# Optimization experiments

Hardware: AMD Instinct MI355X
Metric: run time of the kernel (lower is better)

The kernel has to match this reference:

```python
import jax, jax.numpy as jnp
import numpy as np

N_NODES = 100000
N_EDGES = 1600000
IN_C, HID, OUT_C = 16, 64, 1


def setup_inputs() -> dict:
    key = jax.random.key(0)
    ks = jax.random.split(key, 12)
    x = jax.random.normal(ks[0], (N_NODES, IN_C), dtype=jnp.float32)
    edge_index = jax.random.randint(ks[1], (2, N_EDGES), 0, N_NODES, dtype=jnp.int32)

    def lin(k, fan_in, fan_out):
        s = 1.0 / np.sqrt(fan_in)
        kw, kb = jax.random.split(k)
        W = jax.random.uniform(kw, (fan_in, fan_out), jnp.float32, -s, s)
        b = jax.random.uniform(kb, (fan_out,), jnp.float32, -s, s)
        return W, b

    W0, b0 = lin(ks[2], IN_C, HID)      # node_mlps[0]
    W1, b1 = lin(ks[3], HID, HID)       # node_mlps[1]
    W2, b2 = lin(ks[4], HID, OUT_C)     # node_mlps[2]
    M0, bM0 = lin(ks[5], 2 * HID, HID)  # message_mlps[0] (only one used for num_layers=3)
    return {"x": x, "edge_index": edge_index, "W0": W0, "b0": b0,
            "W1": W1, "b1": b1, "W2": W2, "b2": b2, "M0": M0, "bM0": bM0}


def _message_passing(h, src, dst, M, bM):
    # gather -> concat -> linear -> scatter-add -> degree normalize
    msgs = jnp.concatenate([h[src], h[dst]], axis=1) @ M + bM  # [E, HID]
    agg = jax.ops.segment_sum(msgs, dst, num_segments=N_NODES)  # [N, HID]
    deg = jax.ops.segment_sum(jnp.ones((src.shape[0],), h.dtype), dst,
                              num_segments=N_NODES)
    deg = jnp.clip(deg, 1.0, None)[:, None]
    return agg / deg


def reference(x, edge_index, W0, b0, W1, b1, W2, b2, M0, bM0):
    src, dst = edge_index[0], edge_index[1]
    h = jax.nn.relu(x @ W0 + b0)                  # node_mlps[0] (dropout = eval identity)
    h = h + _message_passing(h, src, dst, M0, bM0)
    h = jax.nn.relu(h @ W1 + b1)                  # node_mlps[1]
    return h @ W2 + b2                            # node_mlps[2], [N, 1]
```

## Files before the change

kernel.cpp:

```cpp
#include <hip/hip_runtime.h>

#define HID 64
#define IN_C 16

typedef __attribute__((ext_vector_type(8))) short short8;
typedef __attribute__((ext_vector_type(4))) float f32x4;

__device__ __forceinline__ float bitsf(unsigned u) { return __uint_as_float(u); }
__device__ __forceinline__ unsigned rne16(float f) {
    unsigned u = __float_as_uint(f);
    return (u + 0x7fffu + ((u >> 16) & 1u)) >> 16;
}
__device__ __forceinline__ float lanebcf(float v, int l) {
    return __int_as_float(__builtin_amdgcn_readlane(__float_as_int(v), l));
}
__device__ __forceinline__ float f4c(const float4& a, int c) {
    switch (c & 3) { case 0: return a.x; case 1: return a.y; case 2: return a.z; default: return a.w; }
}

__global__ void k_init(const float* __restrict__ M0, const float* __restrict__ W1,
                       const float* __restrict__ bM0, const float* __restrict__ b1,
                       ushort* __restrict__ WPhi, ushort* __restrict__ WPlo,
                       float* __restrict__ bias192) {
    int tid = blockIdx.x * 256 + threadIdx.x;
    if (tid >= 64 * 192) return;
    int cc = tid % 192;
    int k  = tid / 192;
    float w;
    if (cc < 64) {
        float a = 0.f;
#pragma unroll
        for (int m = 0; m < HID; ++m) a = fmaf(M0[k * HID + m], W1[m * HID + cc], a);
        w = a;
    } else if (cc < 128) {
        int c = cc - 64;
        float a = W1[k * HID + c];
#pragma unroll
        for (int m = 0; m < HID; ++m) a = fmaf(M0[(HID + k) * HID + m], W1[m * HID + c], a);
        w = a;
    } else {
        w = W1[k * HID + (cc - 128)];
    }
    unsigned wb = __float_as_uint(w);
    ushort hi = (ushort)(wb >> 16);
    float hif = __uint_as_float(wb & 0xffff0000u);
    ushort lo = (ushort)(__float_as_uint(w - hif) >> 16);
    int ct = cc >> 4, s = k >> 5, l = ((k >> 3) & 3) * 16 + (cc & 15), j = k & 7;
    int fi = ((ct * 2 + s) * 64 + l) * 8 + j;
    WPhi[fi] = hi;
    WPlo[fi] = lo;
    if (k == 0) {
        float bv;
        if (cc < 64) bv = 0.f;
        else if (cc < 128) {
            int c = cc - 64;
            float a = b1[c];
#pragma unroll
            for (int m = 0; m < HID; ++m) a = fmaf(bM0[m], W1[m * HID + c], a);
            bv = a;
        } else bv = b1[cc - 128];
        bias192[cc] = bv;
    }
}

__global__ __launch_bounds__(256) void k_pre_hist(
    const float* __restrict__ x, const float* __restrict__ W0, const float* __restrict__ b0,
    const ushort* __restrict__ WPhi, const ushort* __restrict__ WPlo,
    const float* __restrict__ bias192,
    ushort* __restrict__ zb, float* __restrict__ PQ, ushort* __restrict__ Ppb, int N,
    const int* __restrict__ ei, int* __restrict__ bhT, int E, int B1, int NB1)
{
    __shared__ ushort hhi[64 * 64];
    __shared__ ushort hlo[64 * 64];

    if ((int)blockIdx.x < NB1) {
        int* h = reinterpret_cast<int*>(hhi);
        for (int i = threadIdx.x; i < B1; i += 256) h[i] = 0;
        __syncthreads();
        int CH = (E + NB1 - 1) / NB1;
        int e0 = blockIdx.x * CH;
        int e1 = min(e0 + CH, E);
        for (int e = e0 + (int)threadIdx.x; e < e1; e += 256)
            atomicAdd(&h[ei[E + e] >> 8], 1);
        __syncthreads();
        for (int i = threadIdx.x; i < B1; i += 256)
            bhT[(size_t)i * NB1 + blockIdx.x] = h[i];
        return;
    }

    int tid  = threadIdx.x;
    int lane = tid & 63;
    int w    = tid >> 6;
    int n0   = (blockIdx.x - NB1) * 64;

    float w0c[IN_C];
#pragma unroll
    for (int k = 0; k < IN_C; ++k) w0c[k] = W0[k * HID + lane];
    float b0l = b0[lane];

    short8 Whi[3][2], Wlo[3][2];
    float4 bias4[3];
#pragma unroll
    for (int i = 0; i < 3; ++i) {
        int ct = w * 3 + i;
#pragma unroll
        for (int s = 0; s < 2; ++s) {
            int fi = ((ct * 2 + s) * 64 + lane) * 8;
            Whi[i][s] = *reinterpret_cast<const short8*>(WPhi + fi);
            Wlo[i][s] = *reinterpret_cast<const short8*>(WPlo + fi);
        }
        bias4[i] = *reinterpret_cast<const float4*>(bias192 + ct * 16 + (lane >> 4) * 4);
    }

    int nx = n0 + w * 16 + (lane >> 2);
    float4 xq = make_float4(0.f, 0.f, 0.f, 0.f);
    if (nx < N) xq = *reinterpret_cast<const float4*>(x + (size_t)nx * IN_C + (lane & 3) * 4);

#pragma unroll
    for (int nn = 0; nn < 16; ++nn) {
        float acc = b0l;
#pragma unroll
        for (int k = 0; k < IN_C; ++k)
            acc = fmaf(lanebcf(f4c(xq, k & 3), 4 * nn + (k >> 2)), w0c[k], acc);
        float h = fmaxf(acc, 0.f);
        unsigned hb = __float_as_uint(h);
        ushort hi = (ushort)(hb >> 16);
        float hif = __uint_as_float(hb & 0xffff0000u);
        ushort lo = (ushort)(__float_as_uint(h - hif) >> 16);
        int nl = w * 16 + nn;
        int u  = ((lane >> 3) ^ (nl & 7));
        int off = nl * 64 + u * 8 + (lane & 7);
        hhi[off] = hi;
        hlo[off] = lo;
    }
    __syncthreads();

#pragma unroll
    for (int st = 0; st < 4; ++st) {
        int nloc = st * 16 + (lane & 15);
        short8 Ahi[2], Alo[2];
#pragma unroll
        for (int s = 0; s < 2; ++s) {
            int u = (s * 4 + (lane >> 4)) ^ (nloc & 7);
            int off = nloc * 64 + u * 8;
            Ahi[s] = *reinterpret_cast<const short8*>(hhi + off);
            Alo[s] = *reinterpret_cast<const short8*>(hlo + off);
        }
        int n = n0 + st * 16 + (lane & 15);
#pragma unroll
        for (int i = 0; i < 3; ++i) {
            int ct = w * 3 + i;
            f32x4 acc = {bias4[i].x, bias4[i].y, bias4[i].z, bias4[i].w};
#pragma unroll
            for (int s = 0; s < 2; ++s) {
                acc = __builtin_amdgcn_mfma_f32_16x16x32_bf16(Whi[i][s], Ahi[s], acc, 0, 0, 0);
                acc = __builtin_amdgcn_mfma_f32_16x16x32_bf16(Whi[i][s], Alo[s], acc, 0, 0, 0);
                acc = __builtin_amdgcn_mfma_f32_16x16x32_bf16(Wlo[i][s], Ahi[s], acc, 0, 0, 0);
                acc = __builtin_amdgcn_mfma_f32_16x16x32_bf16(Wlo[i][s], Alo[s], acc, 0, 0, 0);
            }
            if (n < N) {
                int chb = ct * 16 + (lane >> 4) * 4;
                if (chb < 64) {
                    uint2 pk;
                    pk.x = rne16(acc[0]) | (rne16(acc[1]) << 16);
                    pk.y = rne16(acc[2]) | (rne16(acc[3]) << 16);
                    *reinterpret_cast<uint2*>(zb + (size_t)n * HID + chb) = pk;
                } else if (chb < 128) {
                    float4 v = make_float4(acc[0], acc[1], acc[2], acc[3]);
                    *reinterpret_cast<float4*>(PQ + (size_t)n * HID + (chb - 64)) = v;
                } else {
                    uint2 pk;
                    pk.x = rne16(acc[0]) | (rne16(acc[1]) << 16);
                    pk.y = rne16(acc[2]) | (rne16(acc[3]) << 16);
                    *reinterpret_cast<uint2*>(Ppb + (size_t)n * HID + (chb - 128)) = pk;
                }
            }
        }
    }
}

__global__ void k_scan1(const int* __restrict__ cnt, int* __restrict__ rs,
                        int* __restrict__ bsum, int M) {
    __shared__ int lds[256];
    int t = threadIdx.x;
    int base = blockIdx.x * 4096 + t * 16;
    int v[16];
    if (base + 16 <= M) {
#pragma unroll
        for (int u = 0; u < 4; ++u) {
            int4 w = *reinterpret_cast<const int4*>(cnt + base + u * 4);
            v[u * 4 + 0] = w.x; v[u * 4 + 1] = w.y; v[u * 4 + 2] = w.z; v[u * 4 + 3] = w.w;
        }
    } else {
#pragma unroll
        for (int u = 0; u < 16; ++u) v[u] = (base + u < M) ? cnt[base + u] : 0;
    }
    int run = 0;
#pragma unroll
    for (int u = 0; u < 16; ++u) { int tv = v[u]; v[u] = run; run += tv; }
    lds[t] = run;
    __syncthreads();
#pragma unroll
    for (int off = 1; off < 256; off <<= 1) {
        int xw = (t >= off) ? lds[t - off] : 0;
        __syncthreads();
        lds[t] += xw;
        __syncthreads();
    }
    int excl = lds[t] - run;
    if (t == 255) bsum[blockIdx.x] = lds[255];
#pragma unroll
    for (int u = 0; u < 16; ++u)
        if (base + u < M) rs[base + u] = excl + v[u];
}

__global__ __launch_bounds__(256) void k_p1scat(const int* __restrict__ ei, const int* __restrict__ off,
                                                const int* __restrict__ bsum, int NBs,
                                                unsigned* __restrict__ tmp, int E, int B1) {
    __shared__ int cur[1024];
    __shared__ int lds[256];
    __shared__ int excl[256];
    int NB1 = gridDim.x;
    int t = threadIdx.x;
    int v = (t < NBs) ? bsum[t] : 0;
    lds[t] = v;
    __syncthreads();
#pragma unroll
    for (int o = 1; o < 256; o <<= 1) {
        int xw = (t >= o) ? lds[t - o] : 0;
        __syncthreads();
        lds[t] += xw;
        __syncthreads();
    }
    excl[t] = lds[t] - v;
    __syncthreads();
    for (int i = t; i < B1; i += 256) {
        int idx = i * NB1 + blockIdx.x;
        cur[i] = off[idx] + excl[idx >> 12];
    }
    __syncthreads();
    int CH = (E + NB1 - 1) / NB1;
    int e0 = blockIdx.x * CH;
    int e1 = min(e0 + CH, E);
    for (int e = e0 + t; e < e1; e += 256) {
        int s = ei[e];
        int d = ei[E + e];
        int pos = atomicAdd(&cur[d >> 8], 1);
        tmp[pos] = (unsigned)s | ((unsigned)(d & 255) << 24);
    }
}

__global__ __launch_bounds__(256) void k_p2(const unsigned* __restrict__ tmp, const int* __restrict__ off,
                                            const int* __restrict__ bsum, int NBs,
                                            int* __restrict__ rs, int* __restrict__ csr,
                                            int E, int N, int B1, int NB1) {
    __shared__ int h2[256];
    __shared__ int sc[256];
    __shared__ int cur[256];
    __shared__ int bb[2];
    int b = blockIdx.x;
    int t = threadIdx.x;

    {
        int v = (t < NBs) ? bsum[t] : 0;
        sc[t] = v;
        __syncthreads();
#pragma unroll
        for (int o = 1; o < 256; o <<= 1) {
            int xw = (t >= o) ? sc[t - o] : 0;
            __syncthreads();
            sc[t] += xw;
            __syncthreads();
        }
        if (t == 0) {
            int i0 = b * NB1;
            bb[0] = off[i0] + (sc[i0 >> 12] - ((i0 >> 12) < NBs ? bsum[i0 >> 12] : 0));
        } else if (t == 1 && b < B1 - 1) {
            int i1 = (b + 1) * NB1;
            bb[1] = off[i1] + (sc[i1 >> 12] - ((i1 >> 12) < NBs ? bsum[i1 >> 12] : 0));
        } else if (t == 1) {
            bb[1] = E;
        }
    }
    __syncthreads();
    int bb0 = bb[0];
    int bb1 = bb[1];

    h2[t] = 0;
    __syncthreads();
    for (int i = bb0 + t; i < bb1; i += 256)
        atomicAdd(&h2[tmp[i] >> 24], 1);
    __syncthreads();

    int v = h2[t];
    sc[t] = v;
    __syncthreads();
#pragma unroll
    for (int o = 1; o < 256; o <<= 1) {
        int xw = (t >= o) ? sc[t - o] : 0;
        __syncthreads();
        sc[t] += xw;
        __syncthreads();
    }
    int excl = sc[t] - v;

    int node = b * 256 + t;
    if (node < N) rs[node] = bb0 + excl;
    if (b == B1 - 1 && t == 0) rs[N] = E;
    cur[t] = bb0 + excl;
    __syncthreads();

    for (int i = bb0 + t; i < bb1; i += 256) {
        unsigned ed = tmp[i];
        int pos = atomicAdd(&cur[ed >> 24], 1);
        csr[pos] = (int)(ed & 0x00FFFFFFu);
    }
}

__global__ __launch_bounds__(256) void k_final(
    const ushort* __restrict__ zb, const float* __restrict__ PQ, const ushort* __restrict__ Ppb,
    const int* __restrict__ rs, const int* __restrict__ csr,
    const float* __restrict__ W2, const float* __restrict__ b2,
    float* __restrict__ out, int N)
{
    int lane = threadIdx.x & 63;
    int g    = lane >> 4;
    int ql   = lane & 15;
    int oct  = ql & 7;
    int half = ql >> 3;
    int wid  = (blockIdx.x * 256 + threadIdx.x) >> 6;
    int nw   = (gridDim.x * 256) >> 6;

    int c0 = oct * 8 + half * 4;
    float4 w2v = *reinterpret_cast<const float4*>(W2 + c0);
    float b2s = b2[0];

    for (int n0 = wid * 4; n0 < N; n0 += nw * 4) {
        int ng   = n0 + g;
        bool okg = ng < N;

        int rv = okg ? rs[ng + half] : 0;
        int beg = __shfl(rv, g * 16 + 0);
        int end = __shfl(rv, g * 16 + 8);
        int deg = end - beg;
        int md = deg;
        md = max(md, __shfl_xor(md, 16));
        md = max(md, __shfl_xor(md, 32));

        float acc[8];
#pragma unroll
        for (int i = 0; i < 8; ++i) acc[i] = 0.f;

        for (int c = 0; c < md; c += 32) {
            int j0 = c + ql, j1 = c + 16 + ql;
            int ia = (j0 < deg) ? csr[beg + j0] : -1;
            int ib = (j1 < deg) ? csr[beg + j1] : -1;
#pragma unroll
            for (int tb = 0; tb < 4; ++tb) {
                if (tb > 0 && md <= c + 8 * tb) break;
                int srcs[4];
#pragma unroll
                for (int t4 = 0; t4 < 4; ++t4) {
                    int t = tb * 4 + t4;
                    int e = 2 * t + half;
                    srcs[t4] = __shfl(tb < 2 ? ia : ib, g * 16 + (e & 15));
                }
                uint4 rw[4];
#pragma unroll
                for (int t4 = 0; t4 < 4; ++t4) {
                    int s = srcs[t4] < 0 ? 0 : srcs[t4];
                    rw[t4] = *reinterpret_cast<const uint4*>(zb + (size_t)s * HID + oct * 8);
                }
#pragma unroll
                for (int t4 = 0; t4 < 4; ++t4) {
                    if (srcs[t4] >= 0) {
                        uint4 wv = rw[t4];
                        acc[0] += bitsf(wv.x << 16); acc[1] += bitsf(wv.x & 0xffff0000u);
                        acc[2] += bitsf(wv.y << 16); acc[3] += bitsf(wv.y & 0xffff0000u);
                        acc[4] += bitsf(wv.z << 16); acc[5] += bitsf(wv.z & 0xffff0000u);
                        acc[6] += bitsf(wv.w << 16); acc[7] += bitsf(wv.w & 0xffff0000u);
                    }
                }
            }
        }
#pragma unroll
        for (int i = 0; i < 8; ++i) acc[i] += __shfl_xor(acc[i], 8);

        float s0 = half ? acc[4] : acc[0];
        float s1 = half ? acc[5] : acc[1];
        float s2 = half ? acc[6] : acc[2];
        float s3 = half ? acc[7] : acc[3];

        float4 base = make_float4(0.f, 0.f, 0.f, 0.f);
        if (okg) {
            base = *reinterpret_cast<const float4*>(PQ + (size_t)ng * HID + c0);
            if (deg == 0) {
                uint2 pb = *reinterpret_cast<const uint2*>(Ppb + (size_t)ng * HID + c0);
                base.x = bitsf(pb.x << 16); base.y = bitsf(pb.x & 0xffff0000u);
                base.z = bitsf(pb.y << 16); base.w = bitsf(pb.y & 0xffff0000u);
            }
        }
        float rcpd = (deg > 0) ? (1.f / (float)deg) : 0.f;
        float y0 = base.x + s0 * rcpd;
        float y1 = base.y + s1 * rcpd;
        float y2 = base.z + s2 * rcpd;
        float y3 = base.w + s3 * rcpd;

        float part = fmaxf(y0, 0.f) * w2v.x + fmaxf(y1, 0.f) * w2v.y +
                     fmaxf(y2, 0.f) * w2v.z + fmaxf(y3, 0.f) * w2v.w;
#pragma unroll
        for (int off = 1; off < 16; off <<= 1) part += __shfl_xor(part, off);
        if (ql == 0 && okg) out[ng] = part + b2s;
    }
}

extern "C" void kernel_launch(void* const* d_in, const int* in_sizes, int n_in,
                              void* d_out, int out_size, void* d_ws, size_t ws_size,
                              hipStream_t stream) {
    const float* x   = (const float*)d_in[0];
    const int*   ei  = (const int*)d_in[1];
    const float* W0  = (const float*)d_in[2];
    const float* b0  = (const float*)d_in[3];
    const float* W1  = (const float*)d_in[4];
    const float* b1  = (const float*)d_in[5];
    const float* W2  = (const float*)d_in[6];
    const float* b2  = (const float*)d_in[7];
    const float* M0  = (const float*)d_in[8];
    const float* bM0 = (const float*)d_in[9];

    int N = in_sizes[0] / IN_C;
    int E = in_sizes[1] / 2;
    int B1 = (N + 255) >> 8;
    int NB1 = 256;
    int M2 = B1 * NB1;
    int NBs = (M2 + 4095) / 4096;

    ushort*   zb     = (ushort*)d_ws;
    float*    PQ     = (float*)(zb + (size_t)N * HID);
    ushort*   Ppb    = (ushort*)(PQ + (size_t)N * HID);
    ushort*   WPhi   = Ppb + (size_t)N * HID;
    ushort*   WPlo   = WPhi + 12288;
    float*    bias192= (float*)(WPlo + 12288);
    int*      bhT    = (int*)(bias192 + 192);
    int*      off    = bhT + (size_t)M2;
    int*      bsum   = off + (size_t)M2;
    int*      rs     = bsum + 256;
    unsigned* tmp    = (unsigned*)(rs + N + 1);
    int*      csr    = (int*)(tmp + (size_t)E);
    float*    out    = (float*)d_out;

    int npre = (N + 63) / 64;

    k_init<<<48, 256, 0, stream>>>(M0, W1, bM0, b1, WPhi, WPlo, bias192);
    k_pre_hist<<<NB1 + npre, 256, 0, stream>>>(x, W0, b0, WPhi, WPlo, bias192,
                                               zb, PQ, Ppb, N, ei, bhT, E, B1, NB1);
    k_scan1<<<NBs, 256, 0, stream>>>(bhT, off, bsum, M2);
    k_p1scat<<<NB1, 256, 0, stream>>>(ei, off, bsum, NBs, tmp, E, B1);
    k_p2<<<B1, 256, 0, stream>>>(tmp, off, bsum, NBs, rs, csr, E, N, B1, NB1);
    k_final<<<2048, 256, 0, stream>>>(zb, PQ, Ppb, rs, csr, W2, b2, out, N);
}
```

Measured before the change: 101.8 us.

## Fuse CSR fine-sort into final aggregation with 64-node buckets and LDS-resident CSR

Shrinks the destination buckets from 256 to 64 nodes and merges the second-pass sort kernel with the final aggregation kernel. Each block now sorts its bucket's edges into a shared-memory CSR and consumes them directly, with a global-memory fallback when a bucket holds more than LCAP edges. The aim is to cut one launch and the global write and re-read of the row-start and CSR arrays. In exchange, the fused grid has fewer blocks than the old final kernel, and each block serializes its sort phase before aggregation.

```diff
diff --git a/kernel.cpp b/kernel.cpp
--- a/kernel.cpp
+++ b/kernel.cpp
@@ -2,6 +2,8 @@
 
 #define HID 64
 #define IN_C 16
+#define BKT 64
+#define LCAP 2048
 
 typedef __attribute__((ext_vector_type(8))) short short8;
 typedef __attribute__((ext_vector_type(4))) float f32x4;
@@ -81,7 +83,7 @@
         int e0 = blockIdx.x * CH;
         int e1 = min(e0 + CH, E);
         for (int e = e0 + (int)threadIdx.x; e < e1; e += 256)
-            atomicAdd(&h[ei[E + e] >> 8], 1);
+            atomicAdd(&h[ei[E + e] >> 6], 1);
         __syncthreads();
         for (int i = threadIdx.x; i < B1; i += 256)
             bhT[(size_t)i * NB1 + blockIdx.x] = h[i];
@@ -217,7 +219,7 @@
 __global__ __launch_bounds__(256) void k_p1scat(const int* __restrict__ ei, const int* __restrict__ off,
                                                 const int* __restrict__ bsum, int NBs,
                                                 unsigned* __restrict__ tmp, int E, int B1) {
-    __shared__ int cur[1024];
+    __shared__ int cur[2048];
     __shared__ int lds[256];
     __shared__ int excl[256];
     int NB1 = gridDim.x;
@@ -245,19 +247,26 @@
     for (int e = e0 + t; e < e1; e += 256) {
         int s = ei[e];
         int d = ei[E + e];
-        int pos = atomicAdd(&cur[d >> 8], 1);
-        tmp[pos] = (unsigned)s | ((unsigned)(d & 255) << 24);
-    }
-}
-
-__global__ __launch_bounds__(256) void k_p2(const unsigned* __restrict__ tmp, const int* __restrict__ off,
-                                            const int* __restrict__ bsum, int NBs,
-                                            int* __restrict__ rs, int* __restrict__ csr,
-                                            int E, int N, int B1, int NB1) {
-    __shared__ int h2[256];
+        int pos = atomicAdd(&cur[d >> 6], 1);
+        tmp[pos] = (unsigned)s | ((unsigned)(d & 63) << 26);
+    }
+}
+
+__global__ __launch_bounds__(256) void k_p2f(
+    const unsigned* __restrict__ tmp, const int* __restrict__ off,
+    const int* __restrict__ bsum, int NBs,
+    const ushort* __restrict__ zb, const float* __restrict__ PQ, const ushort* __restrict__ Ppb,
+    int* __restrict__ gcsr,
+    const float* __restrict__ W2, const float* __restrict__ b2,
+    float* __restrict__ out, int E, int N, int B1, int NB1)
+{
     __shared__ int sc[256];
-    __shared__ int cur[256];
+    __shared__ int h2[BKT];
+    __shared__ int rsl[BKT];
+    __shared__ int cur[BKT];
     __shared__ int bb[2];
+    __shared__ int lcsr[LCAP];
+
     int b = blockIdx.x;
     int t = threadIdx.x;
 
@@ -274,75 +283,75 @@
         }
         if (t == 0) {
             int i0 = b * NB1;
-            bb[0] = off[i0] + (sc[i0 >> 12] - ((i0 >> 12) < NBs ? bsum[i0 >> 12] : 0));
-        } else if (t == 1 && b < B1 - 1) {
-            int i1 = (b + 1) * NB1;
-            bb[1] = off[i1] + (sc[i1 >> 12] - ((i1 >> 12) < NBs ? bsum[i1 >> 12] : 0));
-        } else if (t == 1) {
-            bb[1] = E;
-        }
-    }
-    __syncthreads();
-    int bb0 = bb[0];
-    int bb1 = bb[1];
-
-    h2[t] = 0;
-    __syncthreads();
+            int c = i0 >> 12;
+            bb[0] = off[i0] + (sc[c] - ((c < NBs) ? bsum[c] : 0));
+        }
+        if (t == 1) {
+            if (b < B1 - 1) {
+                int i1 = (b + 1) * NB1;
+                int c = i1 >> 12;
+                bb[1] = off[i1] + (sc[c] - ((c < NBs) ? bsum[c] : 0));
+            } else bb[1] = E;
+        }
+        if (t < BKT) h2[t] = 0;
+    }
+    __syncthreads();
+    int bb0 = bb[0], bb1 = bb[1];
+    bool useg = (bb1 - bb0) > LCAP;
+
     for (int i = bb0 + t; i < bb1; i += 256)
-        atomicAdd(&h2[tmp[i] >> 24], 1);
-    __syncthreads();
-
-    int v = h2[t];
-    sc[t] = v;
-    __syncthreads();
-#pragma unroll
-    for (int o = 1; o < 256; o <<= 1) {
-        int xw = (t >= o) ? sc[t - o] : 0;
-        __syncthreads();
-        sc[t] += xw;
-        __syncthreads();
-    }
-    int excl = sc[t] - v;
-
-    int node = b * 256 + t;
-    if (node < N) rs[node] = bb0 + excl;
-    if (b == B1 - 1 && t == 0) rs[N] = E;
-    cur[t] = bb0 + excl;
-    __syncthreads();
-
-    for (int i = bb0 + t; i < bb1; i += 256) {
-        unsigned ed = tmp[i];
-        int pos = atomicAdd(&cur[ed >> 24], 1);
-        csr[pos] = (int)(ed & 0x00FFFFFFu);
-    }
-}
-
-__global__ __launch_bounds__(256) void k_final(
-    const ushort* __restrict__ zb, const float* __restrict__ PQ, const ushort* __restrict__ Ppb,
-    const int* __restrict__ rs, const int* __restrict__ csr,
-    const float* __restrict__ W2, const float* __restrict__ b2,
-    float* __restrict__ out, int N)
-{
-    int lane = threadIdx.x & 63;
+        atomicAdd(&h2[tmp[i] >> 26], 1);
+    __syncthreads();
+
+    int vdeg = (t < BKT) ? h2[t] : 0;
+    sc[t] = vdeg;
+    __syncthreads();
+#pragma unroll
+    for (int o = 1; o < BKT; o <<= 1) {
+        int xw = (t >= o && t < BKT) ? sc[t - o] : 0;
+        __syncthreads();
+        if (t < BKT) sc[t] += xw;
+        __syncthreads();
+    }
+    if (t < BKT) {
+        int excl = sc[t] - vdeg;
+        rsl[t] = excl;
+        cur[t] = excl;
+    }
+    __syncthreads();
+
+    if (!useg) {
+        for (int i = bb0 + t; i < bb1; i += 256) {
+            unsigned ed = tmp[i];
+            int pos = atomicAdd(&cur[ed >> 26], 1);
+            lcsr[pos] = (int)(ed & 0x03FFFFFFu);
+        }
+    } else {
+        for (int i = bb0 + t; i < bb1; i += 256) {
+            unsigned ed = tmp[i];
+            int pos = atomicAdd(&cur[ed >> 26], 1);
+            gcsr[bb0 + pos] = (int)(ed & 0x03FFFFFFu);
+        }
+    }
+    __syncthreads();
+
+    int lane = t & 63;
+    int w    = t >> 6;
     int g    = lane >> 4;
     int ql   = lane & 15;
     int oct  = ql & 7;
     int half = ql >> 3;
-    int wid  = (blockIdx.x * 256 + threadIdx.x) >> 6;
-    int nw   = (gridDim.x * 256) >> 6;
-
     int c0 = oct * 8 + half * 4;
     float4 w2v = *reinterpret_cast<const float4*>(W2 + c0);
     float b2s = b2[0];
 
-    for (int n0 = wid * 4; n0 < N; n0 += nw * 4) {
-        int ng   = n0 + g;
+#pragma unroll
+    for (int it = 0; it < BKT / 16; ++it) {
+        int nl = it * 16 + w * 4 + g;
+        int ng = b * BKT + nl;
         bool okg = ng < N;
-
-        int rv = okg ? rs[ng + half] : 0;
-        int beg = __shfl(rv, g * 16 + 0);
-        int end = __shfl(rv, g * 16 + 8);
-        int deg = end - beg;
+        int beg = rsl[nl];
+        int deg = h2[nl];
         int md = deg;
         md = max(md, __shfl_xor(md, 16));
         md = max(md, __shfl_xor(md, 32));
@@ -353,16 +362,16 @@
 
         for (int c = 0; c < md; c += 32) {
             int j0 = c + ql, j1 = c + 16 + ql;
-            int ia = (j0 < deg) ? csr[beg + j0] : -1;
-            int ib = (j1 < deg) ? csr[beg + j1] : -1;
+            int ia = (j0 < deg) ? (useg ? gcsr[bb0 + beg + j0] : lcsr[beg + j0]) : -1;
+            int ib = (j1 < deg) ? (useg ? gcsr[bb0 + beg + j1] : lcsr[beg + j1]) : -1;
 #pragma unroll
             for (int tb = 0; tb < 4; ++tb) {
                 if (tb > 0 && md <= c + 8 * tb) break;
                 int srcs[4];
 #pragma unroll
                 for (int t4 = 0; t4 < 4; ++t4) {
-                    int t = tb * 4 + t4;
-                    int e = 2 * t + half;
+                    int tt = tb * 4 + t4;
+                    int e = 2 * tt + half;
                     srcs[t4] = __shfl(tb < 2 ? ia : ib, g * 16 + (e & 15));
                 }
                 uint4 rw[4];
@@ -409,7 +418,7 @@
         float part = fmaxf(y0, 0.f) * w2v.x + fmaxf(y1, 0.f) * w2v.y +
                      fmaxf(y2, 0.f) * w2v.z + fmaxf(y3, 0.f) * w2v.w;
 #pragma unroll
-        for (int off = 1; off < 16; off <<= 1) part += __shfl_xor(part, off);
+        for (int off2 = 1; off2 < 16; off2 <<= 1) part += __shfl_xor(part, off2);
         if (ql == 0 && okg) out[ng] = part + b2s;
     }
 }
@@ -430,7 +439,7 @@
 
     int N = in_sizes[0] / IN_C;
     int E = in_sizes[1] / 2;
-    int B1 = (N + 255) >> 8;
+    int B1 = (N + BKT - 1) >> 6;
     int NB1 = 256;
     int M2 = B1 * NB1;
     int NBs = (M2 + 4095) / 4096;
@@ -444,9 +453,8 @@
     int*      bhT    = (int*)(bias192 + 192);
     int*      off    = bhT + (size_t)M2;
     int*      bsum   = off + (size_t)M2;
-    int*      rs     = bsum + 256;
-    unsigned* tmp    = (unsigned*)(rs + N + 1);
-    int*      csr    = (int*)(tmp + (size_t)E);
+    unsigned* tmp    = (unsigned*)(bsum + 256);
+    int*      gcsr   = (int*)(tmp + (size_t)E);
     float*    out    = (float*)d_out;
 
     int npre = (N + 63) / 64;
@@ -456,6 +464,6 @@
                                                zb, PQ, Ppb, N, ei, bhT, E, B1, NB1);
     k_scan1<<<NBs, 256, 0, stream>>>(bhT, off, bsum, M2);
     k_p1scat<<<NB1, 256, 0, stream>>>(ei, off, bsum, NBs, tmp, E, B1);
-    k_p2<<<B1, 256, 0, stream>>>(tmp, off, bsum, NBs, rs, csr, E, N, B1, NB1);
-    k_final<<<2048, 256, 0, stream>>>(zb, PQ, Ppb, rs, csr, W2, b2, out, N);
-}
+    k_p2f<<<B1, 256, 0, stream>>>(tmp, off, bsum, NBs, zb, PQ, Ppb, gcsr,
+                                  W2, b2, out, E, N, B1, NB1);
+}
```

After: 94.53 us. 7.2% less time.
